# Optimization experiments

Hardware: AMD Instinct MI355X
Metric: run time of the kernel (lower is better)

The kernel has to match this reference:

```python
import jax, jax.numpy as jnp
import numpy as np

B, N, T, F_IN = 32, 512, 12, 128
K, CF, TF, PRED = 3, 64, 64, 12


def _cheb_polys(n, k):
    # identity adjacency -> scaled Laplacian = -I; T0=I, T1=-I, Tk = 2(-I)T_{k-1} - T_{k-2}
    L = -np.eye(n, dtype=np.float32)
    polys = [np.eye(n, dtype=np.float32)]
    if k > 1:
        polys.append(L.copy())
    for i in range(2, k):
        polys.append(2 * L @ polys[i - 1] - polys[i - 2])
    return jnp.asarray(np.stack(polys))  # (K, N, N)


def _conv2d(x, w, b, stride, pad):
    # x: (B,C,H,W), w: (O,I,kh,kw) torch layout
    y = jax.lax.conv_general_dilated(x, w, window_strides=stride, padding=pad,
                                     dimension_numbers=("NCHW", "OIHW", "NCHW"))
    return y + b[None, :, None, None]


def _block(x, cheb, theta, tw, tb, rw, rb, lg, lb, stride):
    # x: (B,N,Fin,T); cheb: (K,N,N); theta: (K,Fin,Fout)
    # fused Chebyshev conv over all t and k: out[b,m,o,t] = sum_{k,n,f} x[b,n,f,t] cheb[k,n,m] theta[k,f,o]
    s = jax.nn.relu(jnp.einsum("bnft,knm,kfo->bmot", x, cheb, theta))  # (B,N,CF,T)
    t = _conv2d(jnp.transpose(s, (0, 2, 1, 3)), tw, tb, (1, stride), ((0, 0), (1, 1)))  # (B,TF,N,T')
    r = _conv2d(jnp.transpose(x, (0, 2, 1, 3)), rw, rb, (1, stride), ((0, 0), (0, 0)))  # (B,TF,N,T')
    h = jnp.transpose(jax.nn.relu(r + t), (0, 3, 2, 1))  # (B,T',N,TF)
    mu = h.mean(-1, keepdims=True)
    var = ((h - mu) ** 2).mean(-1, keepdims=True)
    h = (h - mu) * jax.lax.rsqrt(var + 1e-5) * lg + lb
    return jnp.transpose(h, (0, 2, 3, 1))  # (B,N,TF,T')


def setup_inputs() -> dict:
    key = jax.random.key(0)
    ks = jax.random.split(key, 8)
    rn = lambda k, shape, s=0.05: jax.random.normal(k, shape, dtype=jnp.float32) * s
    return {
        "x": jax.random.normal(ks[0], (B, N, T, F_IN), dtype=jnp.float32),
        "theta0": rn(ks[1], (K, F_IN, CF)),
        "tconv_w0": rn(ks[2], (TF, CF, 1, 3)),
        "tconv_b0": jnp.zeros((TF,), jnp.float32),
        "rconv_w0": rn(ks[3], (TF, F_IN, 1, 1)),
        "rconv_b0": jnp.zeros((TF,), jnp.float32),
        "ln_g0": jnp.ones((TF,), jnp.float32),
        "ln_b0": jnp.zeros((TF,), jnp.float32),
        "theta1": rn(ks[4], (K, TF, CF)),
        "tconv_w1": rn(ks[5], (TF, CF, 1, 3)),
        "tconv_b1": jnp.zeros((TF,), jnp.float32),
        "rconv_w1": rn(ks[6], (TF, TF, 1, 1)),
        "rconv_b1": jnp.zeros((TF,), jnp.float32),
        "ln_g1": jnp.ones((TF,), jnp.float32),
        "ln_b1": jnp.zeros((TF,), jnp.float32),
        "fconv_w": rn(ks[7], (PRED, T, 1, TF)),
        "fconv_b": jnp.zeros((PRED,), jnp.float32),
    }


def reference(x, theta0, tconv_w0, tconv_b0, rconv_w0, rconv_b0, ln_g0, ln_b0,
              theta1, tconv_w1, tconv_b1, rconv_w1, rconv_b1, ln_g1, ln_b1,
              fconv_w, fconv_b):
    cheb = _cheb_polys(x.shape[1], theta0.shape[0])
    h = jnp.transpose(x, (0, 1, 3, 2))  # (B,N,F_in,T)
    h = _block(h, cheb, theta0, tconv_w0, tconv_b0, rconv_w0, rconv_b0, ln_g0, ln_b0, 1)
    h = _block(h, cheb, theta1, tconv_w1, tconv_b1, rconv_w1, rconv_b1, ln_g1, ln_b1, 1)
    hf = jnp.transpose(h, (0, 3, 1, 2))  # (B,T',N,TF)
    out = _conv2d(hf, fconv_w, fconv_b, (1, 1), ((0, 0), (0, 0)))[:, :, :, -1]  # (B,PRED,N)
    return jnp.transpose(out, (0, 2, 1))  # (B,N,PRED)
```

## Files before the change

### kernel.cpp

```cpp
#include <hip/hip_runtime.h>
#include <hip/hip_bf16.h>


typedef __attribute__((ext_vector_type(8))) short bf16x8;
typedef __attribute__((ext_vector_type(4))) float f32x4;

typedef __attribute__((address_space(1))) const unsigned int gu32;
typedef __attribute__((address_space(3))) unsigned int lu32;

#define FR_W1   0
#define FR_TW0  32
#define FR_W2   56
#define FR_TW1  72
#define FR_FW   96
#define N_FRAGS 120

__device__ __forceinline__ unsigned short f2bf(float f) {
    unsigned u = __builtin_bit_cast(unsigned, f);
    return (unsigned short)((u + 0x7FFFu + ((u >> 16) & 1u)) >> 16);
}

__device__ __forceinline__ unsigned short hcvt(float f) {
    union { __hip_bfloat16 h; unsigned short u; } cv;
    cv.h = __float2bfloat16(f);
    return cv.u;
}

template <int CTRL>
__device__ __forceinline__ float dpp_add(float v) {
    int t = __builtin_amdgcn_update_dpp(0, __builtin_bit_cast(int, v),
                                        CTRL, 0xf, 0xf, true);
    return v + __builtin_bit_cast(float, t);
}
__device__ __forceinline__ float red16(float v) {
    v = dpp_add<0xB1>(v);
    v = dpp_add<0x4E>(v);
    v = dpp_add<0x141>(v);
    v = dpp_add<0x140>(v);
    return v;
}

__global__ void prep(const float* __restrict__ th0, const float* __restrict__ tw0,
                     const float* __restrict__ rw0, const float* __restrict__ th1,
                     const float* __restrict__ tw1, const float* __restrict__ rw1,
                     const float* __restrict__ fw,  short* __restrict__ wsb)
{
    int e = blockIdx.x * 256 + threadIdx.x;
    if (e >= N_FRAGS * 512) return;
    int frag = e >> 9;
    int l    = (e >> 3) & 63;
    int i    = e & 7;
    int kif  = ((l >> 4) << 3) + i;
    int nif  = l & 15;
    float val = 0.f;
    if (frag < 32) {
        int ks = frag >> 3, nt = frag & 7;
        int k = ks * 32 + kif, n = nt * 16 + nif;
        if (n < 64) val = th0[k*64+n] - th0[8192 + k*64+n] + th0[16384 + k*64+n];
        else        val = rw0[(n - 64) * 128 + k];
    } else if (frag < 56) {
        int q = frag - 32; int dt = q >> 3, ks = (q >> 2) & 1, nt = q & 3;
        int c = ks * 32 + kif, o = nt * 16 + nif;
        val = tw0[o * 192 + c * 3 + dt];
    } else if (frag < 72) {
        int q = frag - 56; int ks = q >> 3, nt = q & 7;
        int k = ks * 32 + kif, n = nt * 16 + nif;
        if (n < 64) val = th1[k*64+n] - th1[4096 + k*64+n] + th1[8192 + k*64+n];
        else        val = rw1[(n - 64) * 64 + k];
    } else if (frag < 96) {
        int q = frag - 72; int dt = q >> 3, ks = (q >> 2) & 1, nt = q & 3;
        int c = ks * 32 + kif, o = nt * 16 + nif;
        val = tw1[o * 192 + c * 3 + dt];
    } else {
        int ks = frag - 96; int k = ks * 32 + kif; int po = nif;
        val = (po < 12) ? fw[po * 768 + k] : 0.f;
    }
    wsb[e] = (short)f2bf(val);
}

#define LDS_SY(w)  (LDS + (w) * 6144)
#define LDS_WB     (LDS + 24576)

__global__ __launch_bounds__(256, 3) void mstgcn_mfma(
    const float* __restrict__ x,   const short* __restrict__ wsb,
    const float* __restrict__ tb0, const float* __restrict__ rb0,
    const float* __restrict__ lg0, const float* __restrict__ lb0,
    const float* __restrict__ tb1, const float* __restrict__ rb1,
    const float* __restrict__ lg1, const float* __restrict__ lb1,
    const float* __restrict__ fb,  float* __restrict__ out)
{
    __shared__ __align__(16) char LDS[49152];

    const int lane = threadIdx.x & 63;
    const int wave = threadIdx.x >> 6;
    const int l15  = lane & 15;
    const int l4   = lane >> 4;
    const int pair0 = blockIdx.x * 16 + wave * 4;

    char* syB = LDS_SY(wave);
    char* WB  = LDS_WB;

    auto ldwb = [&](int slot) -> bf16x8 {
        return *(const bf16x8*)(WB + slot * 1024 + lane * 16);
    };
    auto stage1 = [&](int slot, int fg) {
        __builtin_amdgcn_global_load_lds(
            (gu32*)(wsb + fg * 512 + lane * 8),
            (lu32*)(WB + slot * 1024), 16, 0, 0);
    };

    int tA[3];
    long gbase[3];
    #pragma unroll
    for (int mt = 0; mt < 3; ++mt) {
        int r = mt * 16 + l15;
        int p = r / 12;
        tA[mt]   = r - p * 12;
        gbase[mt] = ((long)(pair0 + p) * 12 + tA[mt]) * 128;
    }

    #pragma unroll
    for (int i = 0; i < 4; ++i) {
        int sl = i * 4 + wave;
        stage1(sl, ((sl >> 2) << 3) + (sl & 3));
    }
    bf16x8 aC[12];
    #pragma unroll
    for (int ks = 0; ks < 4; ++ks)
        #pragma unroll
        for (int mt = 0; mt < 3; ++mt) {
            const float* p = x + gbase[mt] + ks * 32 + l4 * 8;
            float v[8];
            *(float4*)(v)     = *(const float4*)(p);
            *(float4*)(v + 4) = *(const float4*)(p + 4);
            bf16x8 af;
            #pragma unroll
            for (int j = 0; j < 8; ++j) af[j] = (short)hcvt(v[j]);
            aC[ks * 3 + mt] = af;
        }
    __syncthreads();

    f32x4 acc[3][4];
    #pragma unroll
    for (int mt = 0; mt < 3; ++mt)
        #pragma unroll
        for (int nt = 0; nt < 4; ++nt) acc[mt][nt] = (f32x4)0.f;

    #pragma unroll
    for (int ks = 0; ks < 4; ++ks)
        #pragma unroll
        for (int nt = 0; nt < 4; ++nt) {
            bf16x8 b = ldwb(ks * 4 + nt);
            #pragma unroll
            for (int mt = 0; mt < 3; ++mt)
                acc[mt][nt] = __builtin_amdgcn_mfma_f32_16x16x32_bf16(aC[ks * 3 + mt], b, acc[mt][nt], 0, 0, 0);
        }
    #pragma unroll
    for (int mt = 0; mt < 3; ++mt)
        #pragma unroll
        for (int j = 0; j < 4; ++j) {
            int row = mt * 16 + l4 * 4 + j;
            int sw  = (row & 7) << 4;
            #pragma unroll
            for (int nt = 0; nt < 4; ++nt) {
                int col = nt * 16 + l15;
                *(short*)(syB + row * 128 + ((col * 2) ^ sw)) =
                    (short)hcvt(fmaxf(acc[mt][nt][j], 0.f));
            }
        }
    __syncthreads();

    #pragma unroll
    for (int i = 0; i < 4; ++i) {
        int sl = i * 4 + wave;
        stage1(sl, ((sl >> 2) << 3) + 4 + (sl & 3));
    }
    __syncthreads();

    #pragma unroll
    for (int mt = 0; mt < 3; ++mt)
        #pragma unroll
        for (int nt = 0; nt < 4; ++nt) acc[mt][nt] = (f32x4)0.f;
    #pragma unroll
    for (int ks = 0; ks < 4; ++ks)
        #pragma unroll
        for (int nt = 0; nt < 4; ++nt) {
            bf16x8 b = ldwb(ks * 4 + nt);
            #pragma unroll
            for (int mt = 0; mt < 3; ++mt)
                acc[mt][nt] = __builtin_amdgcn_mfma_f32_16x16x32_bf16(aC[ks * 3 + mt], b, acc[mt][nt], 0, 0, 0);
        }
    __syncthreads();

    #pragma unroll
    for (int i = 0; i < 6; ++i) {
        int sl = i * 4 + wave;
        stage1(sl, FR_TW0 + sl);
    }
    __syncthreads();

    #pragma unroll
    for (int dt = 0; dt < 3; ++dt) {
        #pragma unroll
        for (int ks = 0; ks < 2; ++ks) {
            bf16x8 a[3];
            #pragma unroll
            for (int mt = 0; mt < 3; ++mt) {
                int ts    = tA[mt] + dt - 1;
                bool ok   = (ts >= 0) && (ts < 12);
                int srow  = ok ? (mt * 16 + l15 + dt - 1) : (mt * 16 + l15);
                int kb    = (ks * 32 + l4 * 8) * 2;
                bf16x8 av = *(const bf16x8*)(syB + srow * 128 + (kb ^ ((srow & 7) << 4)));
                a[mt] = ok ? av : (bf16x8)(short)0;
            }
            #pragma unroll
            for (int nt = 0; nt < 4; ++nt) {
                bf16x8 b = ldwb(dt * 8 + ks * 4 + nt);
                #pragma unroll
                for (int mt = 0; mt < 3; ++mt)
                    acc[mt][nt] = __builtin_amdgcn_mfma_f32_16x16x32_bf16(a[mt], b, acc[mt][nt], 0, 0, 0);
            }
        }
    }
    __syncthreads();

    #pragma unroll
    for (int i = 0; i < 4; ++i) {
        int sl = i * 4 + wave;
        stage1(sl, FR_W2 + sl);
    }

    {
        float bv[4], lgv[4], lbv[4];
        #pragma unroll
        for (int nt = 0; nt < 4; ++nt) {
            int col = nt * 16 + l15;
            bv[nt]  = rb0[col] + tb0[col];
            lgv[nt] = lg0[col];
            lbv[nt] = lb0[col];
        }
        #pragma unroll
        for (int mt = 0; mt < 3; ++mt)
            #pragma unroll
            for (int j = 0; j < 4; ++j) {
                float v[4], sm = 0.f, sq = 0.f;
                #pragma unroll
                for (int nt = 0; nt < 4; ++nt) {
                    v[nt] = fmaxf(acc[mt][nt][j] + bv[nt], 0.f);
                    sm += v[nt]; sq += v[nt] * v[nt];
                }
                sm = red16(sm);
                sq = red16(sq);
                float mu = sm * 0.015625f;
                float is = rsqrtf(sq * 0.015625f - mu * mu + 1e-5f);
                int row = mt * 16 + l4 * 4 + j;
                int sw  = (row & 7) << 4;
                #pragma unroll
                for (int nt = 0; nt < 4; ++nt) {
                    int col = nt * 16 + l15;
                    *(short*)(syB + row * 128 + ((col * 2) ^ sw)) =
                        (short)hcvt((v[nt] - mu) * is * lgv[nt] + lbv[nt]);
                }
            }
    }

    bf16x8 aC2[6];
    #pragma unroll
    for (int ks = 0; ks < 2; ++ks)
        #pragma unroll
        for (int mt = 0; mt < 3; ++mt) {
            int row = mt * 16 + l15;
            int kb  = (ks * 32 + l4 * 8) * 2;
            aC2[ks * 3 + mt] = *(const bf16x8*)(syB + row * 128 + (kb ^ ((row & 7) << 4)));
        }
    __syncthreads();

    #pragma unroll
    for (int mt = 0; mt < 3; ++mt)
        #pragma unroll
        for (int nt = 0; nt < 4; ++nt) acc[mt][nt] = (f32x4)0.f;
    #pragma unroll
    for (int ks = 0; ks < 2; ++ks)
        #pragma unroll
        for (int nt = 0; nt < 4; ++nt) {
            bf16x8 b = ldwb(ks * 8 + nt);
            #pragma unroll
            for (int mt = 0; mt < 3; ++mt)
                acc[mt][nt] = __builtin_amdgcn_mfma_f32_16x16x32_bf16(aC2[ks * 3 + mt], b, acc[mt][nt], 0, 0, 0);
        }
    #pragma unroll
    for (int mt = 0; mt < 3; ++mt)
        #pragma unroll
        for (int j = 0; j < 4; ++j) {
            int row = mt * 16 + l4 * 4 + j;
            int sw  = (row & 7) << 4;
            #pragma unroll
            for (int nt = 0; nt < 4; ++nt) {
                int col = nt * 16 + l15;
                *(short*)(syB + row * 128 + ((col * 2) ^ sw)) =
                    (short)hcvt(fmaxf(acc[mt][nt][j], 0.f));
            }
        }

    #pragma unroll
    for (int mt = 0; mt < 3; ++mt)
        #pragma unroll
        for (int nt = 0; nt < 4; ++nt) acc[mt][nt] = (f32x4)0.f;
    #pragma unroll
    for (int ks = 0; ks < 2; ++ks)
        #pragma unroll
        for (int nt = 0; nt < 4; ++nt) {
            bf16x8 b = ldwb(ks * 8 + 4 + nt);
            #pragma unroll
            for (int mt = 0; mt < 3; ++mt)
                acc[mt][nt] = __builtin_amdgcn_mfma_f32_16x16x32_bf16(aC2[ks * 3 + mt], b, acc[mt][nt], 0, 0, 0);
        }
    __syncthreads();

    #pragma unroll
    for (int i = 0; i < 6; ++i) {
        int sl = i * 4 + wave;
        stage1(sl, FR_TW1 + sl);
    }
    __syncthreads();

    #pragma unroll
    for (int dt = 0; dt < 3; ++dt) {
        #pragma unroll
        for (int ks = 0; ks < 2; ++ks) {
            bf16x8 a[3];
            #pragma unroll
            for (int mt = 0; mt < 3; ++mt) {
                int ts    = tA[mt] + dt - 1;
                bool ok   = (ts >= 0) && (ts < 12);
                int srow  = ok ? (mt * 16 + l15 + dt - 1) : (mt * 16 + l15);
                int kb    = (ks * 32 + l4 * 8) * 2;
                bf16x8 av = *(const bf16x8*)(syB + srow * 128 + (kb ^ ((srow & 7) << 4)));
                a[mt] = ok ? av : (bf16x8)(short)0;
            }
            #pragma unroll
            for (int nt = 0; nt < 4; ++nt) {
                bf16x8 b = ldwb(dt * 8 + ks * 4 + nt);
                #pragma unroll
                for (int mt = 0; mt < 3; ++mt)
                    acc[mt][nt] = __builtin_amdgcn_mfma_f32_16x16x32_bf16(a[mt], b, acc[mt][nt], 0, 0, 0);
            }
        }
    }
    __syncthreads();

    #pragma unroll
    for (int i = 0; i < 6; ++i) {
        int sl = i * 4 + wave;
        stage1(sl, FR_FW + sl);
    }

    {
        float bv[4], lgv[4], lbv[4];
        #pragma unroll
        for (int nt = 0; nt < 4; ++nt) {
            int col = nt * 16 + l15;
            bv[nt]  = rb1[col] + tb1[col];
            lgv[nt] = lg1[col];
            lbv[nt] = lb1[col];
        }
        #pragma unroll
        for (int mt = 0; mt < 3; ++mt)
            #pragma unroll
            for (int j = 0; j < 4; ++j) {
                float v[4], sm = 0.f, sq = 0.f;
                #pragma unroll
                for (int nt = 0; nt < 4; ++nt) {
                    v[nt] = fmaxf(acc[mt][nt][j] + bv[nt], 0.f);
                    sm += v[nt]; sq += v[nt] * v[nt];
                }
                sm = red16(sm);
                sq = red16(sq);
                float mu = sm * 0.015625f;
                float is = rsqrtf(sq * 0.015625f - mu * mu + 1e-5f);
                int row = mt * 16 + l4 * 4 + j;
                int sw  = (row & 7) << 4;
                #pragma unroll
                for (int nt = 0; nt < 4; ++nt) {
                    int col = nt * 16 + l15;
                    *(short*)(syB + row * 128 + ((col * 2) ^ sw)) =
                        (short)hcvt((v[nt] - mu) * is * lgv[nt] + lbv[nt]);
                }
            }
    }
    __syncthreads();

    {
        f32x4 acc0 = (f32x4)0.f, acc1 = (f32x4)0.f;
        int p   = (l15 < 4) ? l15 : 0;
        #pragma unroll
        for (int ks = 0; ks < 24; ks += 2) {
            {
                int t = ks >> 1, f0 = l4 * 8;
                int row = p * 12 + t;
                bf16x8 a = *(const bf16x8*)(syB + row * 128 + ((f0 * 2) ^ ((row & 7) << 4)));
                acc0 = __builtin_amdgcn_mfma_f32_16x16x32_bf16(a, ldwb(ks), acc0, 0, 0, 0);
            }
            {
                int t = ks >> 1, f0 = 32 + l4 * 8;
                int row = p * 12 + t;
                bf16x8 a = *(const bf16x8*)(syB + row * 128 + ((f0 * 2) ^ ((row & 7) << 4)));
                acc1 = __builtin_amdgcn_mfma_f32_16x16x32_bf16(a, ldwb(ks + 1), acc1, 0, 0, 0);
            }
        }
        if (l4 == 0 && l15 < 12) {
            float fbv = fb[l15];
            #pragma unroll
            for (int j = 0; j < 4; ++j)
                out[(long)(pair0 + j) * 12 + l15] = acc0[j] + acc1[j] + fbv;
        }
    }
}

extern "C" void kernel_launch(void* const* d_in, const int* in_sizes, int n_in,
                              void* d_out, int out_size, void* d_ws, size_t ws_size,
                              hipStream_t stream)
{
    (void)in_sizes; (void)n_in; (void)out_size; (void)ws_size;
    const float* x   = (const float*)d_in[0];
    const float* th0 = (const float*)d_in[1];
    const float* tw0 = (const float*)d_in[2];
    const float* tb0 = (const float*)d_in[3];
    const float* rw0 = (const float*)d_in[4];
    const float* rb0 = (const float*)d_in[5];
    const float* lg0 = (const float*)d_in[6];
    const float* lb0 = (const float*)d_in[7];
    const float* th1 = (const float*)d_in[8];
    const float* tw1 = (const float*)d_in[9];
    const float* tb1 = (const float*)d_in[10];
    const float* rw1 = (const float*)d_in[11];
    const float* rb1 = (const float*)d_in[12];
    const float* lg1 = (const float*)d_in[13];
    const float* lb1 = (const float*)d_in[14];
    const float* fw  = (const float*)d_in[15];
    const float* fb  = (const float*)d_in[16];
    float* out = (float*)d_out;
    short* wsb = (short*)d_ws;

    prep<<<240, 256, 0, stream>>>(th0, tw0, rw0, th1, tw1, rw1, fw, wsb);
    mstgcn_mfma<<<1024, 256, 0, stream>>>(x, wsb, tb0, rb0, lg0, lb0,
                                          tb1, rb1, lg1, lb1, fb, out);
}
```

Before: 49.16 us.

## Shrink LDS weight buffer and reload x per pass to raise occupancy

Cuts the shared weight staging area from 24 to 16 slots so LDS per block drops to 40KB, and splits the 24-fragment temporal-conv and final-conv weight loads into two staged phases. Instead of keeping all twelve converted x fragments in registers across both Chebyshev GEMM passes, x is reloaded from global and converted per k-step in each pass. Together with launch bounds raised to 4 blocks per CU, this aims to fit more waves per CU. The cost is extra barriers, a duplicate global read of x, and more stage-and-sync round trips.

```diff
diff --git a/kernel.cpp b/kernel.cpp
--- a/kernel.cpp
+++ b/kernel.cpp
@@ -81,7 +81,7 @@
 #define LDS_SY(w)  (LDS + (w) * 6144)
 #define LDS_WB     (LDS + 24576)
 
-__global__ __launch_bounds__(256, 3) void mstgcn_mfma(
+__global__ __launch_bounds__(256, 4) void mstgcn_mfma(
     const float* __restrict__ x,   const short* __restrict__ wsb,
     const float* __restrict__ tb0, const float* __restrict__ rb0,
     const float* __restrict__ lg0, const float* __restrict__ lb0,
@@ -89,7 +89,7 @@
     const float* __restrict__ lg1, const float* __restrict__ lb1,
     const float* __restrict__ fb,  float* __restrict__ out)
 {
-    __shared__ __align__(16) char LDS[49152];
+    __shared__ __align__(16) char LDS[40960];
 
     const int lane = threadIdx.x & 63;
     const int wave = threadIdx.x >> 6;
@@ -103,58 +103,58 @@
     auto ldwb = [&](int slot) -> bf16x8 {
         return *(const bf16x8*)(WB + slot * 1024 + lane * 16);
     };
-    auto stage1 = [&](int slot, int fg) {
+    auto stage = [&](int slot, int fg) {
         __builtin_amdgcn_global_load_lds(
             (gu32*)(wsb + fg * 512 + lane * 8),
             (lu32*)(WB + slot * 1024), 16, 0, 0);
     };
 
     int tA[3];
-    long gbase[3];
     #pragma unroll
     for (int mt = 0; mt < 3; ++mt) {
         int r = mt * 16 + l15;
-        int p = r / 12;
-        tA[mt]   = r - p * 12;
-        gbase[mt] = ((long)(pair0 + p) * 12 + tA[mt]) * 128;
-    }
+        tA[mt] = r - (r / 12) * 12;
+    }
+
+    f32x4 acc[3][4];
+
+    auto ldA = [&](int mt, int ks) -> bf16x8 {
+        int r = mt * 16 + l15;
+        long gb = ((long)(pair0 + r / 12) * 12 + tA[mt]) * 128;
+        const float* pp = x + gb + ks * 32 + l4 * 8;
+        float v[8];
+        *(float4*)(v)     = *(const float4*)(pp);
+        *(float4*)(v + 4) = *(const float4*)(pp + 4);
+        bf16x8 af;
+        #pragma unroll
+        for (int j = 0; j < 8; ++j) af[j] = (short)hcvt(v[j]);
+        return af;
+    };
 
     #pragma unroll
     for (int i = 0; i < 4; ++i) {
         int sl = i * 4 + wave;
-        stage1(sl, ((sl >> 2) << 3) + (sl & 3));
-    }
-    bf16x8 aC[12];
-    #pragma unroll
-    for (int ks = 0; ks < 4; ++ks)
-        #pragma unroll
-        for (int mt = 0; mt < 3; ++mt) {
-            const float* p = x + gbase[mt] + ks * 32 + l4 * 8;
-            float v[8];
-            *(float4*)(v)     = *(const float4*)(p);
-            *(float4*)(v + 4) = *(const float4*)(p + 4);
-            bf16x8 af;
-            #pragma unroll
-            for (int j = 0; j < 8; ++j) af[j] = (short)hcvt(v[j]);
-            aC[ks * 3 + mt] = af;
-        }
-    __syncthreads();
-
-    f32x4 acc[3][4];
+        stage(sl, ((sl >> 2) << 3) + (sl & 3));
+    }
+    __syncthreads();
+
     #pragma unroll
     for (int mt = 0; mt < 3; ++mt)
         #pragma unroll
         for (int nt = 0; nt < 4; ++nt) acc[mt][nt] = (f32x4)0.f;
-
-    #pragma unroll
-    for (int ks = 0; ks < 4; ++ks)
+    #pragma unroll
+    for (int ks = 0; ks < 4; ++ks) {
+        bf16x8 a[3];
+        #pragma unroll
+        for (int mt = 0; mt < 3; ++mt) a[mt] = ldA(mt, ks);
         #pragma unroll
         for (int nt = 0; nt < 4; ++nt) {
             bf16x8 b = ldwb(ks * 4 + nt);
             #pragma unroll
             for (int mt = 0; mt < 3; ++mt)
-                acc[mt][nt] = __builtin_amdgcn_mfma_f32_16x16x32_bf16(aC[ks * 3 + mt], b, acc[mt][nt], 0, 0, 0);
-        }
+                acc[mt][nt] = __builtin_amdgcn_mfma_f32_16x16x32_bf16(a[mt], b, acc[mt][nt], 0, 0, 0);
+        }
+    }
     #pragma unroll
     for (int mt = 0; mt < 3; ++mt)
         #pragma unroll
@@ -173,34 +173,40 @@
     #pragma unroll
     for (int i = 0; i < 4; ++i) {
         int sl = i * 4 + wave;
-        stage1(sl, ((sl >> 2) << 3) + 4 + (sl & 3));
-    }
-    __syncthreads();
+        stage(sl, ((sl >> 2) << 3) + 4 + (sl & 3));
+    }
+    __syncthreads();
+
+    asm volatile("" ::: "memory");
 
     #pragma unroll
     for (int mt = 0; mt < 3; ++mt)
         #pragma unroll
         for (int nt = 0; nt < 4; ++nt) acc[mt][nt] = (f32x4)0.f;
     #pragma unroll
-    for (int ks = 0; ks < 4; ++ks)
+    for (int ks = 0; ks < 4; ++ks) {
+        bf16x8 a[3];
+        #pragma unroll
+        for (int mt = 0; mt < 3; ++mt) a[mt] = ldA(mt, ks);
         #pragma unroll
         for (int nt = 0; nt < 4; ++nt) {
             bf16x8 b = ldwb(ks * 4 + nt);
             #pragma unroll
             for (int mt = 0; mt < 3; ++mt)
-                acc[mt][nt] = __builtin_amdgcn_mfma_f32_16x16x32_bf16(aC[ks * 3 + mt], b, acc[mt][nt], 0, 0, 0);
-        }
-    __syncthreads();
-
-    #pragma unroll
-    for (int i = 0; i < 6; ++i) {
-        int sl = i * 4 + wave;
-        stage1(sl, FR_TW0 + sl);
-    }
-    __syncthreads();
-
-    #pragma unroll
-    for (int dt = 0; dt < 3; ++dt) {
+                acc[mt][nt] = __builtin_amdgcn_mfma_f32_16x16x32_bf16(a[mt], b, acc[mt][nt], 0, 0, 0);
+        }
+    }
+    __syncthreads();
+
+    #pragma unroll
+    for (int i = 0; i < 4; ++i) {
+        int sl = i * 4 + wave;
+        stage(sl, FR_TW0 + sl);
+    }
+    __syncthreads();
+
+    #pragma unroll
+    for (int dt = 0; dt < 2; ++dt) {
         #pragma unroll
         for (int ks = 0; ks < 2; ++ks) {
             bf16x8 a[3];
@@ -225,9 +231,38 @@
     __syncthreads();
 
     #pragma unroll
+    for (int i = 0; i < 2; ++i) {
+        int sl = i * 4 + wave;
+        stage(sl, FR_TW0 + 16 + sl);
+    }
+    __syncthreads();
+
+    #pragma unroll
+    for (int ks = 0; ks < 2; ++ks) {
+        bf16x8 a[3];
+        #pragma unroll
+        for (int mt = 0; mt < 3; ++mt) {
+            int ts    = tA[mt] + 1;
+            bool ok   = (ts < 12);
+            int srow  = ok ? (mt * 16 + l15 + 1) : (mt * 16 + l15);
+            int kb    = (ks * 32 + l4 * 8) * 2;
+            bf16x8 av = *(const bf16x8*)(syB + srow * 128 + (kb ^ ((srow & 7) << 4)));
+            a[mt] = ok ? av : (bf16x8)(short)0;
+        }
+        #pragma unroll
+        for (int nt = 0; nt < 4; ++nt) {
+            bf16x8 b = ldwb(ks * 4 + nt);
+            #pragma unroll
+            for (int mt = 0; mt < 3; ++mt)
+                acc[mt][nt] = __builtin_amdgcn_mfma_f32_16x16x32_bf16(a[mt], b, acc[mt][nt], 0, 0, 0);
+        }
+    }
+    __syncthreads();
+
+    #pragma unroll
     for (int i = 0; i < 4; ++i) {
         int sl = i * 4 + wave;
-        stage1(sl, FR_W2 + sl);
+        stage(sl, FR_W2 + sl);
     }
 
     {
@@ -318,14 +353,14 @@
     __syncthreads();
 
     #pragma unroll
-    for (int i = 0; i < 6; ++i) {
-        int sl = i * 4 + wave;
-        stage1(sl, FR_TW1 + sl);
-    }
-    __syncthreads();
-
-    #pragma unroll
-    for (int dt = 0; dt < 3; ++dt) {
+    for (int i = 0; i < 4; ++i) {
+        int sl = i * 4 + wave;
+        stage(sl, FR_TW1 + sl);
+    }
+    __syncthreads();
+
+    #pragma unroll
+    for (int dt = 0; dt < 2; ++dt) {
         #pragma unroll
         for (int ks = 0; ks < 2; ++ks) {
             bf16x8 a[3];
@@ -350,9 +385,38 @@
     __syncthreads();
 
     #pragma unroll
-    for (int i = 0; i < 6; ++i) {
-        int sl = i * 4 + wave;
-        stage1(sl, FR_FW + sl);
+    for (int i = 0; i < 2; ++i) {
+        int sl = i * 4 + wave;
+        stage(sl, FR_TW1 + 16 + sl);
+    }
+    __syncthreads();
+
+    #pragma unroll
+    for (int ks = 0; ks < 2; ++ks) {
+        bf16x8 a[3];
+        #pragma unroll
+        for (int mt = 0; mt < 3; ++mt) {
+            int ts    = tA[mt] + 1;
+            bool ok   = (ts < 12);
+            int srow  = ok ? (mt * 16 + l15 + 1) : (mt * 16 + l15);
+            int kb    = (ks * 32 + l4 * 8) * 2;
+            bf16x8 av = *(const bf16x8*)(syB + srow * 128 + (kb ^ ((srow & 7) << 4)));
+            a[mt] = ok ? av : (bf16x8)(short)0;
+        }
+        #pragma unroll
+        for (int nt = 0; nt < 4; ++nt) {
+            bf16x8 b = ldwb(ks * 4 + nt);
+            #pragma unroll
+            for (int mt = 0; mt < 3; ++mt)
+                acc[mt][nt] = __builtin_amdgcn_mfma_f32_16x16x32_bf16(a[mt], b, acc[mt][nt], 0, 0, 0);
+        }
+    }
+    __syncthreads();
+
+    #pragma unroll
+    for (int i = 0; i < 4; ++i) {
+        int sl = i * 4 + wave;
+        stage(sl, FR_FW + sl);
     }
 
     {
@@ -390,11 +454,11 @@
     }
     __syncthreads();
 
+    f32x4 acc0 = (f32x4)0.f, acc1 = (f32x4)0.f;
     {
-        f32x4 acc0 = (f32x4)0.f, acc1 = (f32x4)0.f;
-        int p   = (l15 < 4) ? l15 : 0;
-        #pragma unroll
-        for (int ks = 0; ks < 24; ks += 2) {
+        int p = (l15 < 4) ? l15 : 0;
+        #pragma unroll
+        for (int ks = 0; ks < 16; ks += 2) {
             {
                 int t = ks >> 1, f0 = l4 * 8;
                 int row = p * 12 + t;
@@ -406,6 +470,33 @@
                 int row = p * 12 + t;
                 bf16x8 a = *(const bf16x8*)(syB + row * 128 + ((f0 * 2) ^ ((row & 7) << 4)));
                 acc1 = __builtin_amdgcn_mfma_f32_16x16x32_bf16(a, ldwb(ks + 1), acc1, 0, 0, 0);
+            }
+        }
+    }
+    __syncthreads();
+
+    #pragma unroll
+    for (int i = 0; i < 2; ++i) {
+        int sl = i * 4 + wave;
+        stage(sl, FR_FW + 16 + sl);
+    }
+    __syncthreads();
+
+    {
+        int p = (l15 < 4) ? l15 : 0;
+        #pragma unroll
+        for (int ks = 16; ks < 24; ks += 2) {
+            {
+                int t = ks >> 1, f0 = l4 * 8;
+                int row = p * 12 + t;
+                bf16x8 a = *(const bf16x8*)(syB + row * 128 + ((f0 * 2) ^ ((row & 7) << 4)));
+                acc0 = __builtin_amdgcn_mfma_f32_16x16x32_bf16(a, ldwb(ks - 16), acc0, 0, 0, 0);
+            }
+            {
+                int t = ks >> 1, f0 = 32 + l4 * 8;
+                int row = p * 12 + t;
+                bf16x8 a = *(const bf16x8*)(syB + row * 128 + ((f0 * 2) ^ ((row & 7) << 4)));
+                acc1 = __builtin_amdgcn_mfma_f32_16x16x32_bf16(a, ldwb(ks - 15), acc1, 0, 0, 0);
             }
         }
         if (l4 == 0 && l15 < 12) {
```

New measurement: 72.47 us. 1.47x slower.
